# Optimization experiments

Measured on AMD Instinct MI355X. Metric: run time of the kernel, lower is better.

Reference implementation:

```python
import jax, jax.numpy as jnp
import numpy as np

B, N_UNK, M_KNOWN = 8, 8192, 2048
C1, C2 = 256, 256
MLP = [512, 256, 256]
K_ENC = 32
D = MLP[-1]


def setup_inputs() -> dict:
    key = jax.random.key(0)
    ks = jax.random.split(key, 16)
    return {
        "unknown": jax.random.normal(ks[0], (B, N_UNK, 3), jnp.float32),
        "known": jax.random.normal(ks[1], (B, M_KNOWN, 3), jnp.float32),
        "unknow_feats": jax.random.normal(ks[2], (B, C1, N_UNK), jnp.float32),
        "known_feats": jax.random.normal(ks[3], (B, C2, M_KNOWN), jnp.float32),
        "conv_w1": jax.random.normal(ks[4], (MLP[1], MLP[0]), jnp.float32) * 0.05,
        "conv_b1": jnp.zeros((MLP[1],), jnp.float32),
        "bn_g1": jnp.ones((MLP[1],), jnp.float32),
        "bn_b1": jnp.zeros((MLP[1],), jnp.float32),
        "bn_m1": jax.random.normal(ks[5], (MLP[1],), jnp.float32) * 0.01,
        "bn_v1": jax.random.uniform(ks[6], (MLP[1],), jnp.float32, 0.5, 1.5),
        "conv_w2": jax.random.normal(ks[7], (MLP[2], MLP[1]), jnp.float32) * 0.05,
        "conv_b2": jnp.zeros((MLP[2],), jnp.float32),
        "bn_g2": jnp.ones((MLP[2],), jnp.float32),
        "bn_b2": jnp.zeros((MLP[2],), jnp.float32),
        "bn_m2": jax.random.normal(ks[8], (MLP[2],), jnp.float32) * 0.01,
        "bn_v2": jax.random.uniform(ks[9], (MLP[2],), jnp.float32, 0.5, 1.5),
        "enc_codewords": jax.random.normal(ks[10], (K_ENC, D), jnp.float32) * float(1.0 / np.sqrt(K_ENC * D)),
        "enc_scale": jax.random.uniform(ks[11], (K_ENC,), jnp.float32, -1.0, 0.0),
        "lin_w": jax.random.normal(ks[12], (D, D * K_ENC), jnp.float32) * 0.02,
        "lin_b": jnp.zeros((D,), jnp.float32),
    }


def _conv_bn_relu(x, w, b, g, beta, mean, var):
    # 1x1 conv over (B,C,N) == channel GEMM, then BN (inference form), then ReLU
    x = jnp.einsum("oc,bcn->bon", w, x) + b[None, :, None]
    x = g[None, :, None] * (x - mean[None, :, None]) * jax.lax.rsqrt(var + 1e-5)[None, :, None] + beta[None, :, None]
    return jax.nn.relu(x)


def reference(unknown, known, unknow_feats, known_feats,
              conv_w1, conv_b1, bn_g1, bn_b1, bn_m1, bn_v1,
              conv_w2, conv_b2, bn_g2, bn_b2, bn_m2, bn_v2,
              enc_codewords, enc_scale, lin_w, lin_b):
    # ---- three_nn: 3 nearest known points for each unknown point ----
    x2 = jnp.sum(unknown * unknown, axis=-1)            # (B,n)
    y2 = jnp.sum(known * known, axis=-1)                # (B,m)
    d2 = x2[:, :, None] - 2.0 * jnp.einsum("bnc,bmc->bnm", unknown, known) + y2[:, None, :]
    dist = jnp.sqrt(jnp.maximum(d2, 1e-12))             # (B,n,m) Euclidean
    neg_d, idx = jax.lax.top_k(-dist, 3)                # 3 smallest
    dist3 = -neg_d                                      # (B,n,3)
    dist_recip = 1.0 / (dist3 + 1e-8)
    weight = dist_recip / jnp.sum(dist_recip, axis=2, keepdims=True)
    # ---- three_interpolate: gather + weighted sum ----
    gathered = jax.vmap(lambda f, i: f[:, i])(known_feats, idx)   # (B,C2,n,3)
    interp = jnp.einsum("bcnk,bnk->bcn", gathered, weight)        # (B,C2,n)
    feats = jnp.concatenate([interp, unknow_feats], axis=1)       # (B,C2+C1,n)
    # ---- SharedMLP (two 1x1 conv + BN + ReLU layers) ----
    h = _conv_bn_relu(feats, conv_w1, conv_b1, bn_g1, bn_b1, bn_m1, bn_v1)
    h = _conv_bn_relu(h, conv_w2, conv_b2, bn_g2, bn_b2, bn_m2, bn_v2)   # (B,D,n)
    # ---- Encoding layer (soft dictionary assignment, residual aggregate) ----
    X = jnp.swapaxes(h, 1, 2)                                     # (B,n,D)
    c2 = jnp.sum(enc_codewords * enc_codewords, axis=-1)          # (K,)
    xn2 = jnp.sum(X * X, axis=-1)                                 # (B,n)
    # scaled_l2: s_k * ||x - c_k||^2 without materializing (B,n,K,D) residuals
    sl = enc_scale[None, None, :] * (xn2[:, :, None] - 2.0 * jnp.einsum("bnd,kd->bnk", X, enc_codewords) + c2[None, None, :])
    A = jax.nn.softmax(sl, axis=-1)                               # (B,n,K)
    E = jnp.einsum("bnk,bnd->bkd", A, X) - jnp.sum(A, axis=1)[:, :, None] * enc_codewords[None]
    E = jax.nn.relu(E).reshape(E.shape[0], -1)                    # (B,K*D)
    E = E / jnp.maximum(jnp.linalg.norm(E, axis=1, keepdims=True), 1e-12)  # F.normalize
    ctx = jax.nn.sigmoid(E @ lin_w.T + lin_b)                     # (B,D)
    # ---- channel-attention fusion ----
    return h * ctx[:, :, None]                                    # (B,D,n)
```

## Files before the change

kernel.cpp:

```cpp
#include <hip/hip_runtime.h>
#include <stdint.h>

typedef unsigned short u16;
typedef unsigned int u32;
typedef __attribute__((ext_vector_type(8))) short short8;
typedef __attribute__((ext_vector_type(4))) float f32x4;
typedef __attribute__((ext_vector_type(4))) u32 u32x4;

#define B_ 8
#define N_ 8192
#define M_ 2048
#define DD 256
#define KENC 32

#define SC1 0
#define SH1 256
#define SC2 512
#define SH2 768
#define C2OFF 1024
#define SOFF 1056
#define RNOFF 1088

#define OFF_IDX3   0ull
#define OFF_W3     786432ull
#define OFF_FT     1572864ull
#define OFF_H1T    68681728ull
#define OFF_ERELU  102236160ull
#define OFF_PART   102498304ull
#define OFF_CONSTS 102760448ull
#define OFF_CTX    102768640ull
#define OFF_W1D    102776832ull
#define OFF_W2D    103038976ull
#define OFF_CWD    103170048ull
#define OFF_FLAG   103186432ull

__device__ __forceinline__ float bf2f(u16 v){ return __uint_as_float(((u32)v)<<16); }
__device__ __forceinline__ u16 f2bf(float f){
  u32 x = __float_as_uint(f);
  return (u16)((x + 0x7FFFu + ((x>>16)&1u)) >> 16);
}
__device__ __forceinline__ float ldf(const void* p, size_t i, int f){
  return f ? ((const float*)p)[i] : bf2f(((const u16*)p)[i]);
}
__device__ __forceinline__ void gl_lds16(const u16* g, u16* l){
  __builtin_amdgcn_global_load_lds(
      (const __attribute__((address_space(1))) void*)g,
      (__attribute__((address_space(3))) void*)l, 16, 0, 0);
}

__global__ __launch_bounds__(256) void k_detect(const void* v1, int* flagp){
  __shared__ int cntb, cntf;
  int t = threadIdx.x;
  if (t==0){ cntb=0; cntf=0; }
  __syncthreads();
  float vb = bf2f(((const u16*)v1)[t]);
  if (!(vb > 0.4f && vb < 1.6f)) atomicAdd(&cntb, 1);
  if (t < 64){
    float vf = ((const float*)v1)[t];
    if (!(vf > 0.4f && vf < 1.6f)) atomicAdd(&cntf, 1);
  }
  __syncthreads();
  if (t==0) flagp[0] = (cntb > 0 && cntf == 0) ? 1 : 0;
}

__global__ __launch_bounds__(256) void k_convert(
    const void* w1, const void* w2, const void* cwsrc, const int* __restrict__ flagp,
    u16* __restrict__ W1d, u16* __restrict__ W2d, u16* __restrict__ CWd){
  int id = blockIdx.x*256 + threadIdx.x;
  int f = flagp[0];
  if (id < 131072){
    W1d[id] = f ? f2bf(((const float*)w1)[id]) : ((const u16*)w1)[id];
  } else if (id < 196608){
    int j = id - 131072;
    W2d[j] = f ? f2bf(((const float*)w2)[j]) : ((const u16*)w2)[j];
  } else if (id < 204800){
    int j = id - 196608;
    CWd[j] = f ? f2bf(((const float*)cwsrc)[j]) : ((const u16*)cwsrc)[j];
  }
}

__global__ __launch_bounds__(256) void k0_setup(
    const void* cb1, const void* g1, const void* be1, const void* m1, const void* v1,
    const void* cb2, const void* g2, const void* be2, const void* m2, const void* v2,
    const u16* __restrict__ CWd, const void* es, const int* __restrict__ flagp,
    float* __restrict__ consts){
  int t = threadIdx.x;
  int f = flagp[0];
  {
    float g = ldf(g1,t,f), be = ldf(be1,t,f), m = ldf(m1,t,f), v = ldf(v1,t,f), cb = ldf(cb1,t,f);
    float r = 1.f/sqrtf(v + 1e-5f);
    float sc = g*r;
    consts[SC1+t] = sc; consts[SH1+t] = (cb-m)*sc + be;
  }
  {
    float g = ldf(g2,t,f), be = ldf(be2,t,f), m = ldf(m2,t,f), v = ldf(v2,t,f), cb = ldf(cb2,t,f);
    float r = 1.f/sqrtf(v + 1e-5f);
    float sc = g*r;
    consts[SC2+t] = sc; consts[SH2+t] = (cb-m)*sc + be;
  }
  if (t < KENC){
    float s = 0.f;
    for (int d=0; d<DD; d++){ float c = bf2f(CWd[t*DD+d]); s = fmaf(c,c,s); }
    consts[C2OFF+t] = s;
    consts[SOFF+t]  = ldf(es,t,f);
  }
}

__global__ __launch_bounds__(256) void k1_three_nn(
    const void* unknown, const void* known, const int* __restrict__ flagp,
    int* __restrict__ idx3, float* __restrict__ w3){
  __shared__ float4 kp[M_];
  int b = blockIdx.y, t = threadIdx.x;
  int f = flagp[0];
  for (int i=t; i<M_; i+=256){
    size_t o = ((size_t)b*M_ + i)*3;
    float x = ldf(known,o,f), y = ldf(known,o+1,f), z = ldf(known,o+2,f);
    float y2 = __fadd_rn(__fadd_rn(__fmul_rn(x,x), __fmul_rn(y,y)), __fmul_rn(z,z));
    kp[i] = make_float4(x,y,z,y2);
  }
  __syncthreads();
  int qq = t >> 2, sl = t & 3;
  int pid = blockIdx.x*64 + qq;
  size_t uo = ((size_t)b*N_ + pid)*3;
  float ux=ldf(unknown,uo,f), uy=ldf(unknown,uo+1,f), uz=ldf(unknown,uo+2,f);
  float x2 = __fadd_rn(__fadd_rn(__fmul_rn(ux,ux), __fmul_rn(uy,uy)), __fmul_rn(uz,uz));
  float u2x = ux+ux, u2y = uy+uy, u2z = uz+uz;
  float b0=3.4e38f, b1=3.4e38f, b2v=3.4e38f;
  int i0=-1, i1=-1, i2=-1;
  for (int j0=0; j0<512; j0+=4){
    float d[4]; int mi[4];
    #pragma unroll
    for (int u=0; u<4; u++){
      int m = (j0+u)*4 + sl;
      mi[u] = m;
      float4 km = kp[m];
      float dot2 = __fadd_rn(__fadd_rn(__fmul_rn(u2x,km.x), __fmul_rn(u2y,km.y)), __fmul_rn(u2z,km.z));
      d[u] = __fadd_rn(__fsub_rn(x2, dot2), km.w);
    }
    #pragma unroll
    for (int u=0; u<4; u++){
      float d2 = d[u];
      if (__builtin_expect(d2 < b2v, 0)){
        int m = mi[u];
        bool lt0 = d2 < b0, lt1 = d2 < b1;
        b2v = lt1 ? b1 : d2;                     i2 = lt1 ? i1 : m;
        float nb1 = lt0 ? b0 : (lt1 ? d2 : b1);  int ni1 = lt0 ? i0 : (lt1 ? m : i1);
        b0  = lt0 ? d2 : b0;                     i0 = lt0 ? m : i0;
        b1 = nb1; i1 = ni1;
      }
    }
  }
  #pragma unroll
  for (int st=1; st<4; st<<=1){
    float o0=__shfl_xor(b0,st,64), o1=__shfl_xor(b1,st,64), o2=__shfl_xor(b2v,st,64);
    int   j0=__shfl_xor(i0,st,64), j1=__shfl_xor(i1,st,64), j2=__shfl_xor(i2,st,64);
    float dv[3] = {o0,o1,o2}; int jv[3] = {j0,j1,j2};
    #pragma unroll
    for (int e=0; e<3; e++){
      float dd = dv[e]; int jj = jv[e];
      bool lt2 = (dd < b2v) || (dd == b2v && jj < i2);
      if (lt2){
        bool lt0 = (dd < b0) || (dd == b0 && jj < i0);
        bool lt1 = (dd < b1) || (dd == b1 && jj < i1);
        if (lt0){ b2v=b1;i2=i1; b1=b0;i1=i0; b0=dd;i0=jj; }
        else if (lt1){ b2v=b1;i2=i1; b1=dd;i1=jj; }
        else { b2v=dd; i2=jj; }
      }
    }
  }
  if (sl == 0){
    float da = __fsqrt_rn(fmaxf(b0,1e-12f));
    float db = __fsqrt_rn(fmaxf(b1,1e-12f));
    float dc = __fsqrt_rn(fmaxf(b2v,1e-12f));
    float r0 = __fdiv_rn(1.f, __fadd_rn(da,1e-8f));
    float r1 = __fdiv_rn(1.f, __fadd_rn(db,1e-8f));
    float r2 = __fdiv_rn(1.f, __fadd_rn(dc,1e-8f));
    float rs = __fadd_rn(__fadd_rn(r0,r1),r2);
    size_t o = ((size_t)b*N_ + pid)*3;
    idx3[o]=i0; idx3[o+1]=i1; idx3[o+2]=i2;
    w3[o]=__fdiv_rn(r0,rs); w3[o+1]=__fdiv_rn(r1,rs); w3[o+2]=__fdiv_rn(r2,rs);
  }
}

__global__ __launch_bounds__(256) void k2_interp(
    const void* kf, const int* __restrict__ idx3,
    const float* __restrict__ w3, const int* __restrict__ flagp, u16* __restrict__ Ft){
  __shared__ u16 Ls[M_*8];
  int ct = blockIdx.x;
  int rg = blockIdx.y;
  int b = blockIdx.z, t = threadIdx.x;
  int f = flagp[0];
  for (int cp=0; cp<4; cp++){
    int c0 = ct*8 + cp*2;
    size_t base0 = ((size_t)b*DD + c0)*M_;
    size_t base1 = base0 + M_;
    for (int i=t; i<M_; i+=256){
      float f0 = ldf(kf, base0+i, f);
      float f1 = ldf(kf, base1+i, f);
      u32 w = (u32)f2bf(f0) | ((u32)f2bf(f1)<<16);
      *(u32*)(Ls + i*8 + cp*2) = w;
    }
  }
  __syncthreads();
  for (int rep=rg*8; rep<rg*8+8; rep++){
    int pid = rep*256 + t;
    size_t o3 = ((size_t)b*N_ + pid)*3;
    int ia = idx3[o3], ib = idx3[o3+1], ic = idx3[o3+2];
    float wa = w3[o3], wb = w3[o3+1], wc = w3[o3+2];
    short8 va = *(const short8*)(Ls + ia*8);
    short8 vb = *(const short8*)(Ls + ib*8);
    short8 vc = *(const short8*)(Ls + ic*8);
    u32x4 pk;
    #pragma unroll
    for (int cq=0; cq<4; cq++){
      float fa0 = bf2f((u16)va[cq*2]),   fb0 = bf2f((u16)vb[cq*2]),   fc0 = bf2f((u16)vc[cq*2]);
      float fa1 = bf2f((u16)va[cq*2+1]), fb1 = bf2f((u16)vb[cq*2+1]), fc1 = bf2f((u16)vc[cq*2+1]);
      float v0 = fmaf(wc, fc0, fmaf(wb, fb0, wa*fa0));
      float v1 = fmaf(wc, fc1, fmaf(wb, fb1, wa*fa1));
      pk[cq] = (u32)f2bf(v0) | ((u32)f2bf(v1)<<16);
    }
    *(u32x4*)(Ft + ((size_t)b*N_ + pid)*512 + ct*8) = pk;
  }
}

__global__ __launch_bounds__(256) void k2b_transpose_uf(
    const void* uf, const int* __restrict__ flagp, u16* __restrict__ Ft){
  __shared__ u16 Ls[64*72];
  int bx = blockIdx.x, cy = blockIdx.y, b = blockIdx.z, t = threadIdx.x;
  int f = flagp[0];
  {
    int n = t & 63, cg = t >> 6;
    for (int i=0; i<16; i++){
      int c = cg*16 + i;
      Ls[n*72 + c] = f2bf(ldf(uf, ((size_t)b*DD + cy*64 + c)*N_ + bx*64 + n, f));
    }
  }
  __syncthreads();
  int nl = t>>2, cc = t&3;
  u16* dst = Ft + ((size_t)b*N_ + bx*64 + nl)*512 + 256 + cy*64 + cc*16;
  *(u32x4*)dst     = *(const u32x4*)(Ls + nl*72 + cc*16);
  *(u32x4*)(dst+8) = *(const u32x4*)(Ls + nl*72 + cc*16 + 8);
}

__global__ __launch_bounds__(256) void gemm_bn_relu(
    const u16* __restrict__ W, const u16* __restrict__ Fin,
    const float* __restrict__ consts, int sc_off, int sh_off,
    u16* __restrict__ Out, int K){
  __shared__ u16 SM[17408];
  u16* As = SM; u16* Bs = SM + 8192;
  int b = blockIdx.z, ot = blockIdx.y*128, nt = blockIdx.x*128;
  int t = threadIdx.x, wave = t>>6, lane = t&63, ln = lane&15, quad = lane>>4;
  int wo = (wave&1)*64, wn = (wave>>1)*64;
  f32x4 acc[4][4];
  #pragma unroll
  for (int i=0;i<4;i++)
    #pragma unroll
    for (int j=0;j<4;j++) acc[i][j] = (f32x4)0.f;
  const u16* Wp = W + (size_t)ot*K;
  const u16* Fp = Fin + ((size_t)b*N_ + nt)*K;
  for (int kk=0; kk<K; kk+=64){
    #pragma unroll
    for (int i=0;i<4;i++){
      int c = wave*256 + i*64 + lane;
      int r = c>>3, k8 = (c&7) ^ (r&7);
      const u16* gA = Wp + (size_t)r*K + kk + k8*8;
      const u16* gB = Fp + (size_t)r*K + kk + k8*8;
      gl_lds16(gA, As + (size_t)(wave*256 + i*64)*8);
      gl_lds16(gB, Bs + (size_t)(wave*256 + i*64)*8);
    }
    __syncthreads();
    #pragma unroll
    for (int kh=0; kh<2; kh++){
      short8 af[4], bfr[4];
      #pragma unroll
      for (int i=0;i<4;i++){
        int R = wo + i*16 + ln, C = kh*4 + quad;
        af[i] = *(const short8*)(As + (size_t)(R*8 + (C^(R&7)))*8);
      }
      #pragma unroll
      for (int j=0;j<4;j++){
        int R = wn + j*16 + ln, C = kh*4 + quad;
        bfr[j] = *(const short8*)(Bs + (size_t)(R*8 + (C^(R&7)))*8);
      }
      #pragma unroll
      for (int i=0;i<4;i++)
        #pragma unroll
        for (int j=0;j<4;j++)
          acc[i][j] = __builtin_amdgcn_mfma_f32_16x16x32_bf16(af[i], bfr[j], acc[i][j], 0,0,0);
    }
    __syncthreads();
  }
  u16* Cs = SM;
  #pragma unroll
  for (int i=0;i<4;i++){
    #pragma unroll
    for (int r=0;r<4;r++){
      int ol = wo + i*16 + quad*4 + r;
      float sc = consts[sc_off + ot + ol], sh = consts[sh_off + ot + ol];
      #pragma unroll
      for (int j=0;j<4;j++){
        float v = fmaxf(fmaf(acc[i][j][r], sc, sh), 0.f);
        Cs[(wn + j*16 + ln)*136 + ol] = f2bf(v);
      }
    }
  }
  __syncthreads();
  int nl = t>>1, half = t&1;
  u16* dst = Out + ((size_t)b*N_ + nt + nl)*256 + ot + half*64;
  const u16* srcr = Cs + nl*136 + half*64;
  #pragma unroll
  for (int c=0;c<8;c++)
    *(u32x4*)(dst + c*8) = *(const u32x4*)(srcr + c*8);
}

__global__ __launch_bounds__(256, 6) void k5_enc_partial(
    const u16* __restrict__ X, const u16* __restrict__ cw,
    const float* __restrict__ consts, float* __restrict__ Epart,
    float* __restrict__ Asum){
  __shared__ u16 Xs[64*256];
  __shared__ float A_lds[64*32];
  int g = blockIdx.x, b = blockIdx.y, t = threadIdx.x;
  int wave = t>>6, lane = t&63, ln = lane&15, quad = lane>>4;
  int ka = lane>>1, h = lane&1;
  int dbase = wave*64 + h*32;
  float c2v0 = consts[C2OFF + ln], c2v1 = consts[C2OFF + 16 + ln];
  float sv0  = consts[SOFF + ln],  sv1  = consts[SOFF + 16 + ln];
  int n0 = g*64;
  const u16* Xp = X + ((size_t)b*N_ + n0)*256;
  #pragma unroll
  for (int i=0;i<8;i++){
    int ch = t + i*256;
    int r = ch>>5, cc = ch&31;
    *(u32x4*)(Xs + r*256 + ((cc ^ (r&15))<<3)) = *(const u32x4*)(Xp + r*256 + cc*8);
  }
  __syncthreads();
  float xnf;
  {
    int row = t>>2, part = t&3;
    float s = 0.f;
    #pragma unroll
    for (int j=0;j<8;j++){
      int cc = part*8 + j;
      short8 xv = *(const short8*)(Xs + row*256 + ((cc ^ (row&15))<<3));
      #pragma unroll
      for (int q=0;q<8;q++){ float x = bf2f((u16)xv[q]); s = fmaf(x,x,s); }
    }
    s += __shfl_xor(s,1,64);
    s += __shfl_xor(s,2,64);
    xnf = s;
  }
  f32x4 pj0 = (f32x4)0.f, pj1 = (f32x4)0.f;
  {
    int row = wave*16 + ln;
    #pragma unroll
    for (int kk=0; kk<256; kk+=32){
      int cc = (kk>>3) + quad;
      short8 a   = *(const short8*)(Xs + row*256 + ((cc ^ (row&15))<<3));
      short8 bf0 = *(const short8*)(cw + (size_t)ln*256 + kk + quad*8);
      short8 bf1 = *(const short8*)(cw + (size_t)(16+ln)*256 + kk + quad*8);
      pj0 = __builtin_amdgcn_mfma_f32_16x16x32_bf16(a, bf0, pj0, 0,0,0);
      pj1 = __builtin_amdgcn_mfma_f32_16x16x32_bf16(a, bf1, pj1, 0,0,0);
    }
  }
  #pragma unroll
  for (int r=0;r<4;r++){
    int nl = wave*16 + quad*4 + r;
    float xv = __shfl(xnf, (quad*4 + r)*4, 64);
    float v0 = sv0 * __fadd_rn(__fsub_rn(xv, __fmul_rn(2.f,pj0[r])), c2v0);
    float v1 = sv1 * __fadd_rn(__fsub_rn(xv, __fmul_rn(2.f,pj1[r])), c2v1);
    float mx = fmaxf(v0,v1);
    #pragma unroll
    for (int d=1; d<16; d<<=1) mx = fmaxf(mx, __shfl_xor(mx, d, 64));
    float e0 = __expf(v0-mx), e1 = __expf(v1-mx);
    float es = e0+e1;
    #pragma unroll
    for (int d=1; d<16; d<<=1) es += __shfl_xor(es, d, 64);
    float inv = 1.f/es;
    A_lds[nl*32 + ln]      = e0*inv;
    A_lds[nl*32 + 16 + ln] = e1*inv;
  }
  __syncthreads();
  float accE[32];
  #pragma unroll
  for (int p=0;p<32;p++) accE[p]=0.f;
  float asum = 0.f;
  int cbase = wave*8 + h*4;
  #pragma unroll 2
  for (int n=0; n<64; n++){
    float a = A_lds[n*32 + ka];
    asum += a;
    const u16* xr = Xs + n*256;
    int sw = (n&15)<<3;
    #pragma unroll
    for (int p8=0; p8<4; p8++){
      u32x4 xv = *(const u32x4*)(xr + ((((cbase + p8)<<3) ^ sw)));
      #pragma unroll
      for (int q=0; q<4; q++){
        u32 w = xv[q];
        float lo = __uint_as_float(w<<16);
        float hi = __uint_as_float(w & 0xffff0000u);
        accE[p8*8 + q*2]   = fmaf(a, lo, accE[p8*8 + q*2]);
        accE[p8*8 + q*2+1] = fmaf(a, hi, accE[p8*8 + q*2+1]);
      }
    }
  }
  int slab = b*128 + g;
  float* Ed = Epart + (size_t)slab*8192 + (size_t)ka*256 + dbase;
  #pragma unroll
  for (int p=0;p<32;p++) Ed[p] = accE[p];
  if (wave==0 && h==0) Asum[slab*32 + ka] = asum;
}

__global__ __launch_bounds__(256) void k5b_reduce(
    const float* __restrict__ Epart, const float* __restrict__ Asum,
    const u16* __restrict__ cw, float* __restrict__ Erelu){
  int id = blockIdx.x*256 + threadIdx.x;
  int d = id & 255, k = (id>>8)&31, b = id>>13;
  float s = 0.f, as = 0.f;
  for (int sl=0; sl<128; sl++){
    s  += Epart[((size_t)(b*128+sl))*8192 + (size_t)k*256 + d];
    as += Asum[(b*128+sl)*32 + k];
  }
  float cv = bf2f(cw[k*256+d]);
  Erelu[(size_t)b*8192 + k*256 + d] = fmaxf(s - as*cv, 0.f);
}

__global__ __launch_bounds__(256) void k6a_norm(
    const float* __restrict__ Erelu, float* __restrict__ consts){
  __shared__ float red[256];
  int b = blockIdx.x, t = threadIdx.x;
  float s = 0.f;
  for (int i=0;i<32;i++){ float e = Erelu[(size_t)b*8192 + i*256 + t]; s = fmaf(e,e,s); }
  red[t] = s; __syncthreads();
  for (int w=128; w>0; w>>=1){ if (t<w) red[t] += red[t+w]; __syncthreads(); }
  if (t==0) consts[RNOFF + b] = 1.f/fmaxf(__fsqrt_rn(red[0]), 1e-12f);
}

__global__ __launch_bounds__(256) void k6b_partial(
    const float* __restrict__ Erelu, const void* lw, const int* __restrict__ flagp,
    float* __restrict__ partials){
  __shared__ float Er[256];
  int kc = blockIdx.x, b = blockIdx.y, t = threadIdx.x;
  int f = flagp[0];
  Er[t] = Erelu[(size_t)b*8192 + kc*256 + t];
  __syncthreads();
  float s = 0.f;
  if (f){
    const float* lwp = (const float*)lw + (size_t)t*8192 + kc*256;
    for (int p=0; p<256; p+=4){
      f32x4 v = *(const f32x4*)(lwp + p);
      #pragma unroll
      for (int q=0;q<4;q++) s = fmaf(Er[p+q], v[q], s);
    }
  } else {
    const u16* lwp = (const u16*)lw + (size_t)t*8192 + kc*256;
    for (int p=0; p<256; p+=8){
      u32x4 v = *(const u32x4*)(lwp + p);
      #pragma unroll
      for (int q=0;q<4;q++){
        u32 w = v[q];
        s = fmaf(Er[p+q*2],   __uint_as_float(w<<16), s);
        s = fmaf(Er[p+q*2+1], __uint_as_float(w & 0xffff0000u), s);
      }
    }
  }
  partials[((size_t)b*32 + kc)*256 + t] = s;
}

__global__ __launch_bounds__(256) void k6c_ctx(
    const float* __restrict__ partials, const float* __restrict__ consts,
    const void* lb, const int* __restrict__ flagp, float* __restrict__ ctx){
  int b = blockIdx.x, t = threadIdx.x;
  int f = flagp[0];
  float s = 0.f;
  for (int kc=0; kc<32; kc++) s += partials[((size_t)b*32+kc)*256 + t];
  float x = fmaf(consts[RNOFF+b], s, ldf(lb,t,f));
  ctx[b*256 + t] = 1.f/(1.f + __expf(-x));
}

__global__ __launch_bounds__(256) void k7_out(
    const u16* __restrict__ ht, const float* __restrict__ ctx,
    const int* __restrict__ flagp, void* out){
  __shared__ u16 Ls[64*72];
  int bx = blockIdx.x, oy = blockIdx.y, b = blockIdx.z, t = threadIdx.x;
  int f = flagp[0];
  {
    int nl = t>>2, oc = t&3;
    const u16* src = ht + ((size_t)b*N_ + bx*64 + nl)*256 + oy*64 + oc*16;
    *(u32x4*)(Ls + nl*72 + oc*16)     = *(const u32x4*)src;
    *(u32x4*)(Ls + nl*72 + oc*16 + 8) = *(const u32x4*)(src + 8);
  }
  __syncthreads();
  int ol = t>>2, nc = t&3;
  float cv = ctx[b*256 + oy*64 + ol];
  size_t dstoff = ((size_t)b*DD + oy*64 + ol)*N_ + bx*64 + nc*16;
  if (f){
    float* dst = (float*)out + dstoff;
    #pragma unroll
    for (int wq=0; wq<4; wq++){
      f32x4 v;
      #pragma unroll
      for (int q=0;q<4;q++) v[q] = bf2f(Ls[(nc*16 + wq*4 + q)*72 + ol]) * cv;
      *(f32x4*)(dst + wq*4) = v;
    }
  } else {
    u32 words[8];
    #pragma unroll
    for (int wq=0; wq<8; wq++){
      float v0 = bf2f(Ls[(nc*16 + wq*2)*72 + ol]) * cv;
      float v1 = bf2f(Ls[(nc*16 + wq*2+1)*72 + ol]) * cv;
      words[wq] = (u32)f2bf(v0) | ((u32)f2bf(v1)<<16);
    }
    u16* dst = (u16*)out + dstoff;
    u32x4 w0 = {words[0],words[1],words[2],words[3]};
    u32x4 w1 = {words[4],words[5],words[6],words[7]};
    *(u32x4*)dst     = w0;
    *(u32x4*)(dst+8) = w1;
  }
}

extern "C" void kernel_launch(void* const* d_in, const int* in_sizes, int n_in,
                              void* d_out, int out_size, void* d_ws, size_t ws_size,
                              hipStream_t stream){
  const void* unknown = d_in[0];
  const void* known   = d_in[1];
  const void* uf      = d_in[2];
  const void* kf      = d_in[3];
  const void* w1      = d_in[4];
  const void* cb1     = d_in[5];
  const void* g1      = d_in[6];
  const void* be1     = d_in[7];
  const void* m1      = d_in[8];
  const void* v1      = d_in[9];
  const void* w2      = d_in[10];
  const void* cb2     = d_in[11];
  const void* g2      = d_in[12];
  const void* be2     = d_in[13];
  const void* m2      = d_in[14];
  const void* v2      = d_in[15];
  const void* cw      = d_in[16];
  const void* es      = d_in[17];
  const void* lw      = d_in[18];
  const void* lb      = d_in[19];

  char* ws = (char*)d_ws;
  int*   idx3  = (int*)(ws + OFF_IDX3);
  float* w3    = (float*)(ws + OFF_W3);
  u16*   Ft    = (u16*)(ws + OFF_FT);
  u16*   ht    = Ft;
  u16*   h1t   = (u16*)(ws + OFF_H1T);
  float* Epart = (float*)(ws + OFF_H1T);
  float* Asum  = (float*)(ws + OFF_IDX3);
  float* Erelu    = (float*)(ws + OFF_ERELU);
  float* partials = (float*)(ws + OFF_PART);
  float* consts   = (float*)(ws + OFF_CONSTS);
  float* ctx      = (float*)(ws + OFF_CTX);
  u16*   W1d   = (u16*)(ws + OFF_W1D);
  u16*   W2d   = (u16*)(ws + OFF_W2D);
  u16*   CWd   = (u16*)(ws + OFF_CWD);
  int*   flagp = (int*)(ws + OFF_FLAG);

  k_detect<<<1, 256, 0, stream>>>(v1, flagp);
  k_convert<<<800, 256, 0, stream>>>(w1, w2, cw, flagp, W1d, W2d, CWd);
  k0_setup<<<1, 256, 0, stream>>>(cb1,g1,be1,m1,v1, cb2,g2,be2,m2,v2, CWd, es, flagp, consts);
  k1_three_nn<<<dim3(128,8), 256, 0, stream>>>(unknown, known, flagp, idx3, w3);
  k2_interp<<<dim3(32,4,8), 256, 0, stream>>>(kf, idx3, w3, flagp, Ft);
  k2b_transpose_uf<<<dim3(128,4,8), 256, 0, stream>>>(uf, flagp, Ft);
  gemm_bn_relu<<<dim3(64,2,8), 256, 0, stream>>>(W1d, Ft,  consts, SC1, SH1, h1t, 512);
  gemm_bn_relu<<<dim3(64,2,8), 256, 0, stream>>>(W2d, h1t, consts, SC2, SH2, ht,  256);
  k5_enc_partial<<<dim3(128,8), 256, 0, stream>>>(ht, CWd, consts, Epart, Asum);
  k5b_reduce<<<256, 256, 0, stream>>>(Epart, Asum, CWd, Erelu);
  k6a_norm<<<8, 256, 0, stream>>>(Erelu, consts);
  k6b_partial<<<dim3(32,8), 256, 0, stream>>>(Erelu, lw, flagp, partials);
  k6c_ctx<<<8, 256, 0, stream>>>(partials, consts, lb, flagp, ctx);
  k7_out<<<dim3(128,4,8), 256, 0, stream>>>(ht, ctx, flagp, d_out);
}
```

Before: 446.1 us.

## Use branchless med3 top-3 distance pass then thresholded index recovery pass

The three_nn kernel now first finds the 3 smallest distances without indices, using fmin/fmed3 sorting-network updates with no divergent branches. A second pass over the LDS-resident known points recomputes the distances and only does the index-tracking insertion when a group's minimum is at or below the third-best threshold. This removes warp divergence and index bookkeeping from the hot loop, at the cost of computing every distance twice. Tie-breaking by lowest index is kept explicitly in the second pass.

```diff
diff --git a/kernel.cpp b/kernel.cpp
--- a/kernel.cpp
+++ b/kernel.cpp
@@ -106,6 +106,10 @@
   }
 }
 
+__device__ __forceinline__ float k1_dist2(float x2, float u2x, float u2y, float u2z, float4 km){
+  float dot2 = __fadd_rn(__fadd_rn(__fmul_rn(u2x,km.x), __fmul_rn(u2y,km.y)), __fmul_rn(u2z,km.z));
+  return __fadd_rn(__fsub_rn(x2, dot2), km.w);
+}
 __global__ __launch_bounds__(256) void k1_three_nn(
     const void* unknown, const void* known, const int* __restrict__ flagp,
     int* __restrict__ idx3, float* __restrict__ w3){
@@ -126,52 +130,81 @@
   float x2 = __fadd_rn(__fadd_rn(__fmul_rn(ux,ux), __fmul_rn(uy,uy)), __fmul_rn(uz,uz));
   float u2x = ux+ux, u2y = uy+uy, u2z = uz+uz;
   float b0=3.4e38f, b1=3.4e38f, b2v=3.4e38f;
-  int i0=-1, i1=-1, i2=-1;
+  const float4* kpl = kp + sl;
   for (int j0=0; j0<512; j0+=4){
-    float d[4]; int mi[4];
     #pragma unroll
     for (int u=0; u<4; u++){
-      int m = (j0+u)*4 + sl;
-      mi[u] = m;
-      float4 km = kp[m];
-      float dot2 = __fadd_rn(__fadd_rn(__fmul_rn(u2x,km.x), __fmul_rn(u2y,km.y)), __fmul_rn(u2z,km.z));
-      d[u] = __fadd_rn(__fsub_rn(x2, dot2), km.w);
-    }
-    #pragma unroll
-    for (int u=0; u<4; u++){
-      float d2 = d[u];
-      if (__builtin_expect(d2 < b2v, 0)){
-        int m = mi[u];
-        bool lt0 = d2 < b0, lt1 = d2 < b1;
-        b2v = lt1 ? b1 : d2;                     i2 = lt1 ? i1 : m;
-        float nb1 = lt0 ? b0 : (lt1 ? d2 : b1);  int ni1 = lt0 ? i0 : (lt1 ? m : i1);
-        b0  = lt0 ? d2 : b0;                     i0 = lt0 ? m : i0;
-        b1 = nb1; i1 = ni1;
-      }
+      float4 km = kpl[(j0+u)*4];
+      float d2 = k1_dist2(x2,u2x,u2y,u2z,km);
+      float t0 = fminf(b0, d2);
+      float t1 = __builtin_amdgcn_fmed3f(b0, b1, d2);
+      float t2 = __builtin_amdgcn_fmed3f(b1, b2v, d2);
+      b0=t0; b1=t1; b2v=t2;
     }
   }
   #pragma unroll
   for (int st=1; st<4; st<<=1){
     float o0=__shfl_xor(b0,st,64), o1=__shfl_xor(b1,st,64), o2=__shfl_xor(b2v,st,64);
+    float dv[3] = {o0,o1,o2};
+    #pragma unroll
+    for (int e=0; e<3; e++){
+      float dd = dv[e];
+      float t0 = fminf(b0, dd);
+      float t1 = __builtin_amdgcn_fmed3f(b0, b1, dd);
+      float t2 = __builtin_amdgcn_fmed3f(b1, b2v, dd);
+      b0=t0; b1=t1; b2v=t2;
+    }
+  }
+  float T = b2v;
+  float e0=3.4e38f, e1=3.4e38f, e2=3.4e38f;
+  int i0=0x7fffffff, i1=0x7fffffff, i2=0x7fffffff;
+  for (int j0=0; j0<512; j0+=4){
+    float d[4];
+    #pragma unroll
+    for (int u=0; u<4; u++){
+      float4 km = kpl[(j0+u)*4];
+      d[u] = k1_dist2(x2,u2x,u2y,u2z,km);
+    }
+    float gmin = fminf(fminf(d[0],d[1]), fminf(d[2],d[3]));
+    if (__builtin_expect(gmin <= T, 0)){
+      #pragma unroll
+      for (int u=0; u<4; u++){
+        float dd = d[u];
+        if (dd <= T){
+          int m = (j0+u)*4 + sl;
+          bool lt0 = (dd < e0) || (dd == e0 && m < i0);
+          bool lt1 = (dd < e1) || (dd == e1 && m < i1);
+          bool lt2 = (dd < e2) || (dd == e2 && m < i2);
+          float n2 = lt1 ? e1 : (lt2 ? dd : e2);  int ni2 = lt1 ? i1 : (lt2 ? m : i2);
+          float n1 = lt0 ? e0 : (lt1 ? dd : e1);  int ni1 = lt0 ? i0 : (lt1 ? m : i1);
+          e0 = lt0 ? dd : e0;  i0 = lt0 ? m : i0;
+          e1 = n1; i1 = ni1; e2 = n2; i2 = ni2;
+        }
+      }
+    }
+  }
+  #pragma unroll
+  for (int st=1; st<4; st<<=1){
+    float o0=__shfl_xor(e0,st,64), o1=__shfl_xor(e1,st,64), o2=__shfl_xor(e2,st,64);
     int   j0=__shfl_xor(i0,st,64), j1=__shfl_xor(i1,st,64), j2=__shfl_xor(i2,st,64);
     float dv[3] = {o0,o1,o2}; int jv[3] = {j0,j1,j2};
     #pragma unroll
     for (int e=0; e<3; e++){
       float dd = dv[e]; int jj = jv[e];
-      bool lt2 = (dd < b2v) || (dd == b2v && jj < i2);
+      bool lt2 = (dd < e2) || (dd == e2 && jj < i2);
       if (lt2){
-        bool lt0 = (dd < b0) || (dd == b0 && jj < i0);
-        bool lt1 = (dd < b1) || (dd == b1 && jj < i1);
-        if (lt0){ b2v=b1;i2=i1; b1=b0;i1=i0; b0=dd;i0=jj; }
-        else if (lt1){ b2v=b1;i2=i1; b1=dd;i1=jj; }
-        else { b2v=dd; i2=jj; }
+        bool lt0 = (dd < e0) || (dd == e0 && jj < i0);
+        bool lt1 = (dd < e1) || (dd == e1 && jj < i1);
+        if (lt0){ e2=e1;i2=i1; e1=e0;i1=i0; e0=dd;i0=jj; }
+        else if (lt1){ e2=e1;i2=i1; e1=dd;i1=jj; }
+        else { e2=dd; i2=jj; }
       }
     }
   }
   if (sl == 0){
-    float da = __fsqrt_rn(fmaxf(b0,1e-12f));
-    float db = __fsqrt_rn(fmaxf(b1,1e-12f));
-    float dc = __fsqrt_rn(fmaxf(b2v,1e-12f));
+    float da = __fsqrt_rn(fmaxf(e0,1e-12f));
+    float db = __fsqrt_rn(fmaxf(e1,1e-12f));
+    float dc = __fsqrt_rn(fmaxf(e2,1e-12f));
     float r0 = __fdiv_rn(1.f, __fadd_rn(da,1e-8f));
     float r1 = __fdiv_rn(1.f, __fadd_rn(db,1e-8f));
     float r2 = __fdiv_rn(1.f, __fadd_rn(dc,1e-8f));
```

Measured after the change: 472.4 us. +5.9%, slower.
